# Kernel optimization log

Measured on AMD Instinct MI355X. Metric: run time of the kernel, lower is better.

Reference implementation:

```python
import jax, jax.numpy as jnp
import numpy as np

# --- tree topology: complete binary tree, C = 2^(D+1)-1 nodes ---
K = 2           # branching factor
DEPTH = 10      # levels 0..DEPTH
C = 2 ** (DEPTH + 1) - 1   # 2047 classes
L = 4           # n_labels
B = 512         # batch size

_PARENT = (np.arange(C) - 1) // K          # parent index; node 0 is root
# nodes at depth d: [k^d - 1, k^(d+1) - 1) for k=2 -> [2^d-1, 2^(d+1)-1)
_LEVELS = [np.arange(2 ** d - 1, 2 ** (d + 1) - 1) for d in range(DEPTH + 1)]


def setup_inputs() -> dict:
    key = jax.random.key(0)
    k1, k2 = jax.random.split(key)
    X = jax.random.normal(k1, (B, C, L), dtype=jnp.float32)
    # torch.nn.init.uniform_(pairs, 0.1, 1.0)
    pairs = jax.random.uniform(k2, (C, C, L, L), dtype=jnp.float32,
                               minval=0.1, maxval=1.0)
    return {"X": X, "pairs": pairs}


def _upward(X, pairs):
    # alphas[b, i, y_i] = sum over children j of logsumexp_{y_j}(pairs[i,j,y_i,y_j] + X[b,j,y_j] + alphas[b,j,y_j])
    alphas = jnp.zeros((B, C, L), dtype=X.dtype)
    for d in range(DEPTH, 0, -1):          # leaves -> root (reversed BFS)
        nodes = _LEVELS[d]                 # children at this depth
        par = _PARENT[nodes]
        local = X[:, nodes, :] + alphas[:, nodes, :]        # (B, n, L_j)
        trans = pairs[par, nodes]                            # (n, L_i, L_j)
        msg = jax.nn.logsumexp(trans[None, :, :, :] + local[:, :, None, :], axis=-1)  # (B, n, L_i)
        alphas = alphas.at[:, par, :].add(msg)               # duplicate parents accumulate
    return alphas


def _downward(X, pairs):
    # betas[b, i, y_i] = logsumexp_{y_j}(pairs[i,j,y_i,y_j] + X[b,j,y_j] + betas[b,j,y_j]), j = parent(i)
    betas = jnp.zeros((B, C, L), dtype=X.dtype)
    for d in range(1, DEPTH + 1):          # root -> leaves (BFS)
        nodes = _LEVELS[d]                 # children receiving messages
        par = _PARENT[nodes]
        local = X[:, par, :] + betas[:, par, :]              # (B, n, L_j)
        trans = pairs[nodes, par]                            # (n, L_i, L_j): child-first index
        msg = jax.nn.logsumexp(trans[None, :, :, :] + local[:, :, None, :], axis=-1)
        betas = betas.at[:, nodes, :].add(msg)
    return betas


def reference(X, pairs):
    alphas = _upward(X, pairs)
    betas = _downward(X, pairs)
    logits = X + alphas + betas
    return jax.nn.log_softmax(logits, axis=-1)   # logits - logsumexp over labels
```

## Files before the change

kernel.cpp:

```cpp
#include <hip/hip_runtime.h>
#include <cstddef>

namespace {

constexpr int B     = 512;
constexpr int C     = 2047;
constexpr int L     = 4;
constexpr int BLOCK = 256;
constexpr int NINT  = 1023;

__device__ __forceinline__ float4 ld4(const float* p) {
    return *reinterpret_cast<const float4*>(p);
}
__device__ __forceinline__ void st4f(float* p, const float4 v) {
    *reinterpret_cast<float4*>(p) = v;
}
__device__ __forceinline__ float4 add4(const float4 a, const float4 b) {
    float4 r; r.x = a.x + b.x; r.y = a.y + b.y; r.z = a.z + b.z; r.w = a.w + b.w;
    return r;
}

__device__ __forceinline__ float lse4(float v0, float v1, float v2, float v3) {
    const float m = fmaxf(fmaxf(v0, v1), fmaxf(v2, v3));
    const float s = __expf(v0 - m) + __expf(v1 - m) + __expf(v2 - m) + __expf(v3 - m);
    return m + __logf(s);
}

__device__ __forceinline__ void write_lsm(float* __restrict__ o, const float4 g) {
    const float z = lse4(g.x, g.y, g.z, g.w);
    float4 r; r.x = g.x - z; r.y = g.y - z; r.z = g.z - z; r.w = g.w - z;
    st4f(o, r);
}

__device__ __forceinline__ float4 up2(const float* __restrict__ pairs, int p,
                                      const float4 lc0, const float4 lc1) {
    const int c0 = 2 * p + 1;
    const float* __restrict__ t = pairs + ((size_t)p * C + c0) * 16;
    float4 acc;
    {
        const float4 a = ld4(t + 0), bq = ld4(t + 16);
        acc.x = lse4(a.x + lc0.x, a.y + lc0.y, a.z + lc0.z, a.w + lc0.w)
              + lse4(bq.x + lc1.x, bq.y + lc1.y, bq.z + lc1.z, bq.w + lc1.w);
    }
    {
        const float4 a = ld4(t + 4), bq = ld4(t + 20);
        acc.y = lse4(a.x + lc0.x, a.y + lc0.y, a.z + lc0.z, a.w + lc0.w)
              + lse4(bq.x + lc1.x, bq.y + lc1.y, bq.z + lc1.z, bq.w + lc1.w);
    }
    {
        const float4 a = ld4(t + 8), bq = ld4(t + 24);
        acc.z = lse4(a.x + lc0.x, a.y + lc0.y, a.z + lc0.z, a.w + lc0.w)
              + lse4(bq.x + lc1.x, bq.y + lc1.y, bq.z + lc1.z, bq.w + lc1.w);
    }
    {
        const float4 a = ld4(t + 12), bq = ld4(t + 28);
        acc.w = lse4(a.x + lc0.x, a.y + lc0.y, a.z + lc0.z, a.w + lc0.w)
              + lse4(bq.x + lc1.x, bq.y + lc1.y, bq.z + lc1.z, bq.w + lc1.w);
    }
    return acc;
}

__device__ __forceinline__ float4 dn_msg(const float* __restrict__ pairs,
                                         int c, int p, const float4 lp) {
    const float* __restrict__ t = pairs + ((size_t)c * C + p) * 16;
    const float4 t0 = ld4(t + 0), t1 = ld4(t + 4), t2 = ld4(t + 8), t3 = ld4(t + 12);
    float4 m;
    m.x = lse4(t0.x + lp.x, t0.y + lp.y, t0.z + lp.z, t0.w + lp.w);
    m.y = lse4(t1.x + lp.x, t1.y + lp.y, t1.z + lp.z, t1.w + lp.w);
    m.z = lse4(t2.x + lp.x, t2.y + lp.y, t2.z + lp.z, t2.w + lp.w);
    m.w = lse4(t3.x + lp.x, t3.y + lp.y, t3.z + lp.z, t3.w + lp.w);
    return m;
}

__global__ __launch_bounds__(BLOCK, 2) void treecrf_kernel(
    const float* __restrict__ X,
    const float* __restrict__ pairs,
    float* __restrict__ out)
{
    __shared__ float alphas[NINT * L];
    __shared__ float fbo[512 * L];
    __shared__ float fbe[256 * L];
    __shared__ float fbA[32 * L];
    __shared__ float fbB[64 * L];

    const int b   = blockIdx.x;
    const int tid = threadIdx.x;
    const float* __restrict__ Xb = X + (size_t)b * (C * L);
    float* __restrict__ Ob       = out + (size_t)b * (C * L);

    {
        int p = 511 + tid;
        const float4 l0 = ld4(Xb + (2 * p + 1) * L);
        const float4 l1 = ld4(Xb + (2 * p + 2) * L);
        int q = p + 256;
        const float4 m0 = ld4(Xb + (2 * q + 1) * L);
        const float4 m1 = ld4(Xb + (2 * q + 2) * L);
        st4f(&alphas[p * L], up2(pairs, p, l0, l1));
        st4f(&alphas[q * L], up2(pairs, q, m0, m1));
    }
    __syncthreads();

    {
        const int p  = 255 + tid;
        const int c0 = 2 * p + 1;
        const float4 l0 = add4(ld4(Xb + c0 * L), ld4(&alphas[c0 * L]));
        const float4 l1 = add4(ld4(Xb + (c0 + 1) * L), ld4(&alphas[(c0 + 1) * L]));
        st4f(&alphas[p * L], up2(pairs, p, l0, l1));
    }
    __syncthreads();

    if (tid < 128) {
        const int p  = 127 + tid;
        const int c0 = 2 * p + 1;
        const float4 l0 = add4(ld4(Xb + c0 * L), ld4(&alphas[c0 * L]));
        const float4 l1 = add4(ld4(Xb + (c0 + 1) * L), ld4(&alphas[(c0 + 1) * L]));
        st4f(&alphas[p * L], up2(pairs, p, l0, l1));
    }
    __syncthreads();

    if (tid < 64) {
        #pragma unroll 1
        for (int pn = 64; pn >= 1; pn >>= 1) {
            if (tid < pn) {
                const int p  = pn - 1 + tid;
                const int c0 = 2 * p + 1;
                const float4 l0 = add4(ld4(Xb + c0 * L), ld4(&alphas[c0 * L]));
                const float4 l1 = add4(ld4(Xb + (c0 + 1) * L), ld4(&alphas[(c0 + 1) * L]));
                st4f(&alphas[p * L], up2(pairs, p, l0, l1));
            }
            __builtin_amdgcn_wave_barrier();
        }

        const float4 x0 = ld4(Xb);
        if (tid == 0) {
            write_lsm(Ob, add4(x0, ld4(&alphas[0])));
        }
        if (tid < 2) {
            const int c = 1 + tid;
            const float4 m = dn_msg(pairs, c, 0, x0);
            st4f(&fbA[tid * L], m);
            write_lsm(Ob + c * L,
                      add4(add4(ld4(Xb + c * L), ld4(&alphas[c * L])), m));
        }
        __builtin_amdgcn_wave_barrier();

        #pragma unroll 1
        for (int d = 2; d <= 6; ++d) {
            const int n     = 1 << d;
            const int base  = n - 1;
            const int pbase = (1 << (d - 1)) - 1;
            const float* __restrict__ pb = (d & 1) ? fbB : fbA;
            float* __restrict__       cb = (d & 1) ? fbA : fbB;
            if (tid < n) {
                const int c = base + tid;
                const int p = (c - 1) >> 1;
                const float4 lp = add4(ld4(Xb + p * L), ld4(&pb[(p - pbase) * L]));
                const float4 m  = dn_msg(pairs, c, p, lp);
                st4f(&cb[tid * L], m);
                write_lsm(Ob + c * L,
                          add4(add4(ld4(Xb + c * L), ld4(&alphas[c * L])), m));
            }
            __builtin_amdgcn_wave_barrier();
        }
    }
    __syncthreads();

    if (tid < 128) {
        const int c = 127 + tid;
        const int p = (c - 1) >> 1;
        const float4 lp = add4(ld4(Xb + p * L), ld4(&fbB[(p - 63) * L]));
        const float4 m  = dn_msg(pairs, c, p, lp);
        st4f(&fbo[tid * L], m);
        write_lsm(Ob + c * L, add4(add4(ld4(Xb + c * L), ld4(&alphas[c * L])), m));
    }
    __syncthreads();

    {
        const int c = 255 + tid;
        const int p = (c - 1) >> 1;
        const float4 lp = add4(ld4(Xb + p * L), ld4(&fbo[(p - 127) * L]));
        const float4 m  = dn_msg(pairs, c, p, lp);
        st4f(&fbe[tid * L], m);
        write_lsm(Ob + c * L, add4(add4(ld4(Xb + c * L), ld4(&alphas[c * L])), m));
    }
    __syncthreads();

    #pragma unroll
    for (int k = 0; k < 2; ++k) {
        const int idx = tid + k * 256;
        const int c   = 511 + idx;
        const int p   = (c - 1) >> 1;
        const float4 lp = add4(ld4(Xb + p * L), ld4(&fbe[(p - 255) * L]));
        const float4 m  = dn_msg(pairs, c, p, lp);
        st4f(&fbo[idx * L], m);
        write_lsm(Ob + c * L, add4(add4(ld4(Xb + c * L), ld4(&alphas[c * L])), m));
    }
    __syncthreads();

    #pragma unroll
    for (int k = 0; k < 4; ++k) {
        const int idx = tid + k * 256;
        const int c   = 1023 + idx;
        const int p   = (c - 1) >> 1;
        const float4 lp = add4(ld4(Xb + p * L), ld4(&fbo[(p - 511) * L]));
        const float4 m  = dn_msg(pairs, c, p, lp);
        write_lsm(Ob + c * L, add4(ld4(Xb + c * L), m));
    }
}

}

extern "C" void kernel_launch(void* const* d_in, const int* in_sizes, int n_in,
                              void* d_out, int out_size, void* d_ws, size_t ws_size,
                              hipStream_t stream) {
    (void)in_sizes; (void)n_in; (void)out_size; (void)d_ws; (void)ws_size;
    const float* X     = (const float*)d_in[0];
    const float* pairs = (const float*)d_in[1];
    float* out         = (float*)d_out;
    treecrf_kernel<<<B, BLOCK, 0, stream>>>(X, pairs, out);
}
```

Before: 34.59 us.

## Partition tree into per-wave subtrees to replace block barriers with wave barriers

Assigns each of the four wavefronts its own quarter of the tree (the subtree below depth 2), so both the upward and downward sweeps over the lower levels synchronize only within a wave instead of across the whole block. Only the top few levels still use block-wide barriers, handled by a single wave. Shared buffers are also restructured to hold X+alpha and X+beta sums, which removes repeated global X reloads and the ping-pong buffers. The cost is many idle lanes at the shallow levels inside each wave, and correctness depends on the subtree indexing being exactly right.

```diff
diff --git a/kernel.cpp b/kernel.cpp
--- a/kernel.cpp
+++ b/kernel.cpp
@@ -34,8 +34,7 @@
 
 __device__ __forceinline__ float4 up2(const float* __restrict__ pairs, int p,
                                       const float4 lc0, const float4 lc1) {
-    const int c0 = 2 * p + 1;
-    const float* __restrict__ t = pairs + ((size_t)p * C + c0) * 16;
+    const float* __restrict__ t = pairs + ((size_t)p * C + (2 * p + 1)) * 16;
     float4 acc;
     {
         const float4 a = ld4(t + 0), bq = ld4(t + 16);
@@ -77,133 +76,103 @@
     const float* __restrict__ pairs,
     float* __restrict__ out)
 {
-    __shared__ float alphas[NINT * L];
-    __shared__ float fbo[512 * L];
-    __shared__ float fbe[256 * L];
-    __shared__ float fbA[32 * L];
-    __shared__ float fbB[64 * L];
+    __shared__ float la[NINT * L];
+    __shared__ float lb[NINT * L];
 
-    const int b   = blockIdx.x;
-    const int tid = threadIdx.x;
+    const int b    = blockIdx.x;
+    const int tid  = threadIdx.x;
+    const int w    = tid >> 6;
+    const int lane = tid & 63;
     const float* __restrict__ Xb = X + (size_t)b * (C * L);
     float* __restrict__ Ob       = out + (size_t)b * (C * L);
 
-    {
-        int p = 511 + tid;
-        const float4 l0 = ld4(Xb + (2 * p + 1) * L);
-        const float4 l1 = ld4(Xb + (2 * p + 2) * L);
-        int q = p + 256;
-        const float4 m0 = ld4(Xb + (2 * q + 1) * L);
-        const float4 m1 = ld4(Xb + (2 * q + 2) * L);
-        st4f(&alphas[p * L], up2(pairs, p, l0, l1));
-        st4f(&alphas[q * L], up2(pairs, q, m0, m1));
+    #pragma unroll
+    for (int k = 0; k < 2; ++k) {
+        const int p  = 511 + w * 128 + lane + 64 * k;
+        const int c0 = 2 * p + 1;
+        const float4 l0 = ld4(Xb + c0 * L);
+        const float4 l1 = ld4(Xb + (c0 + 1) * L);
+        const float4 a  = up2(pairs, p, l0, l1);
+        st4f(&la[p * L], add4(ld4(Xb + p * L), a));
     }
-    __syncthreads();
+    __builtin_amdgcn_wave_barrier();
 
-    {
-        const int p  = 255 + tid;
-        const int c0 = 2 * p + 1;
-        const float4 l0 = add4(ld4(Xb + c0 * L), ld4(&alphas[c0 * L]));
-        const float4 l1 = add4(ld4(Xb + (c0 + 1) * L), ld4(&alphas[(c0 + 1) * L]));
-        st4f(&alphas[p * L], up2(pairs, p, l0, l1));
-    }
-    __syncthreads();
-
-    if (tid < 128) {
-        const int p  = 127 + tid;
-        const int c0 = 2 * p + 1;
-        const float4 l0 = add4(ld4(Xb + c0 * L), ld4(&alphas[c0 * L]));
-        const float4 l1 = add4(ld4(Xb + (c0 + 1) * L), ld4(&alphas[(c0 + 1) * L]));
-        st4f(&alphas[p * L], up2(pairs, p, l0, l1));
+    #pragma unroll 1
+    for (int dp = 8; dp >= 2; --dp) {
+        const int cnt = 1 << (dp - 2);
+        if (lane < cnt) {
+            const int p  = ((1 << dp) - 1) + w * cnt + lane;
+            const int c0 = 2 * p + 1;
+            const float4 l0 = ld4(&la[c0 * L]);
+            const float4 l1 = ld4(&la[(c0 + 1) * L]);
+            const float4 a  = up2(pairs, p, l0, l1);
+            st4f(&la[p * L], add4(ld4(Xb + p * L), a));
+        }
+        __builtin_amdgcn_wave_barrier();
     }
     __syncthreads();
 
     if (tid < 64) {
-        #pragma unroll 1
-        for (int pn = 64; pn >= 1; pn >>= 1) {
-            if (tid < pn) {
-                const int p  = pn - 1 + tid;
-                const int c0 = 2 * p + 1;
-                const float4 l0 = add4(ld4(Xb + c0 * L), ld4(&alphas[c0 * L]));
-                const float4 l1 = add4(ld4(Xb + (c0 + 1) * L), ld4(&alphas[(c0 + 1) * L]));
-                st4f(&alphas[p * L], up2(pairs, p, l0, l1));
-            }
-            __builtin_amdgcn_wave_barrier();
-        }
-
-        const float4 x0 = ld4(Xb);
-        if (tid == 0) {
-            write_lsm(Ob, add4(x0, ld4(&alphas[0])));
-        }
-        if (tid < 2) {
-            const int c = 1 + tid;
-            const float4 m = dn_msg(pairs, c, 0, x0);
-            st4f(&fbA[tid * L], m);
-            write_lsm(Ob + c * L,
-                      add4(add4(ld4(Xb + c * L), ld4(&alphas[c * L])), m));
+        if (lane < 2) {
+            const int p = 1 + lane;
+            const float4 l0 = ld4(&la[(2 * p + 1) * L]);
+            const float4 l1 = ld4(&la[(2 * p + 2) * L]);
+            const float4 a  = up2(pairs, p, l0, l1);
+            st4f(&la[p * L], add4(ld4(Xb + p * L), a));
         }
         __builtin_amdgcn_wave_barrier();
-
-        #pragma unroll 1
-        for (int d = 2; d <= 6; ++d) {
-            const int n     = 1 << d;
-            const int base  = n - 1;
-            const int pbase = (1 << (d - 1)) - 1;
-            const float* __restrict__ pb = (d & 1) ? fbB : fbA;
-            float* __restrict__       cb = (d & 1) ? fbA : fbB;
-            if (tid < n) {
-                const int c = base + tid;
-                const int p = (c - 1) >> 1;
-                const float4 lp = add4(ld4(Xb + p * L), ld4(&pb[(p - pbase) * L]));
-                const float4 m  = dn_msg(pairs, c, p, lp);
-                st4f(&cb[tid * L], m);
-                write_lsm(Ob + c * L,
-                          add4(add4(ld4(Xb + c * L), ld4(&alphas[c * L])), m));
-            }
-            __builtin_amdgcn_wave_barrier();
+        if (lane == 0) {
+            const float4 l0 = ld4(&la[1 * L]);
+            const float4 l1 = ld4(&la[2 * L]);
+            const float4 a  = up2(pairs, 0, l0, l1);
+            const float4 x0 = ld4(Xb);
+            write_lsm(Ob, add4(x0, a));
+            st4f(&lb[0], x0);
+        }
+        __builtin_amdgcn_wave_barrier();
+        if (lane < 2) {
+            const int c = 1 + lane;
+            const float4 m = dn_msg(pairs, c, 0, ld4(&lb[0]));
+            st4f(&lb[c * L], add4(ld4(Xb + c * L), m));
+            write_lsm(Ob + c * L, add4(ld4(&la[c * L]), m));
+        }
+        __builtin_amdgcn_wave_barrier();
+        if (lane < 4) {
+            const int c = 3 + lane;
+            const int p = (c - 1) >> 1;
+            const float4 m = dn_msg(pairs, c, p, ld4(&lb[p * L]));
+            st4f(&lb[c * L], add4(ld4(Xb + c * L), m));
+            write_lsm(Ob + c * L, add4(ld4(&la[c * L]), m));
         }
     }
     __syncthreads();
 
-    if (tid < 128) {
-        const int c = 127 + tid;
-        const int p = (c - 1) >> 1;
-        const float4 lp = add4(ld4(Xb + p * L), ld4(&fbB[(p - 63) * L]));
-        const float4 m  = dn_msg(pairs, c, p, lp);
-        st4f(&fbo[tid * L], m);
-        write_lsm(Ob + c * L, add4(add4(ld4(Xb + c * L), ld4(&alphas[c * L])), m));
+    #pragma unroll 1
+    for (int dc = 3; dc <= 8; ++dc) {
+        const int cnt = 1 << (dc - 2);
+        if (lane < cnt) {
+            const int c = ((1 << dc) - 1) + w * cnt + lane;
+            const int p = (c - 1) >> 1;
+            const float4 m = dn_msg(pairs, c, p, ld4(&lb[p * L]));
+            st4f(&lb[c * L], add4(ld4(Xb + c * L), m));
+            write_lsm(Ob + c * L, add4(ld4(&la[c * L]), m));
+        }
+        __builtin_amdgcn_wave_barrier();
     }
-    __syncthreads();
-
-    {
-        const int c = 255 + tid;
-        const int p = (c - 1) >> 1;
-        const float4 lp = add4(ld4(Xb + p * L), ld4(&fbo[(p - 127) * L]));
-        const float4 m  = dn_msg(pairs, c, p, lp);
-        st4f(&fbe[tid * L], m);
-        write_lsm(Ob + c * L, add4(add4(ld4(Xb + c * L), ld4(&alphas[c * L])), m));
-    }
-    __syncthreads();
-
     #pragma unroll
     for (int k = 0; k < 2; ++k) {
-        const int idx = tid + k * 256;
-        const int c   = 511 + idx;
-        const int p   = (c - 1) >> 1;
-        const float4 lp = add4(ld4(Xb + p * L), ld4(&fbe[(p - 255) * L]));
-        const float4 m  = dn_msg(pairs, c, p, lp);
-        st4f(&fbo[idx * L], m);
-        write_lsm(Ob + c * L, add4(add4(ld4(Xb + c * L), ld4(&alphas[c * L])), m));
+        const int c = 511 + w * 128 + lane + 64 * k;
+        const int p = (c - 1) >> 1;
+        const float4 m = dn_msg(pairs, c, p, ld4(&lb[p * L]));
+        st4f(&lb[c * L], add4(ld4(Xb + c * L), m));
+        write_lsm(Ob + c * L, add4(ld4(&la[c * L]), m));
     }
-    __syncthreads();
-
+    __builtin_amdgcn_wave_barrier();
     #pragma unroll
     for (int k = 0; k < 4; ++k) {
-        const int idx = tid + k * 256;
-        const int c   = 1023 + idx;
-        const int p   = (c - 1) >> 1;
-        const float4 lp = add4(ld4(Xb + p * L), ld4(&fbo[(p - 511) * L]));
-        const float4 m  = dn_msg(pairs, c, p, lp);
+        const int c = 1023 + w * 256 + lane + 64 * k;
+        const int p = (c - 1) >> 1;
+        const float4 m = dn_msg(pairs, c, p, ld4(&lb[p * L]));
         write_lsm(Ob + c * L, add4(ld4(Xb + c * L), m));
     }
 }
```

Measured after the change: 35.43 us. 2.4% more time.
